# Kernel optimization log

Measured on AMD Instinct MI355X. Metric: run time of the kernel, lower is better.

Reference implementation:

```python
import jax, jax.numpy as jnp
import numpy as np

B, IN, H, G, WR = 8192, 1024, 1024, 2, 64
UR = [64, 64]


def setup_inputs() -> dict:
    key = jax.random.key(0)
    ks = jax.random.split(key, 9)
    hg = H // G
    return {
        "x": jax.random.normal(ks[0], (B, IN), jnp.float32),
        "h": jax.random.normal(ks[1], (B, H), jnp.float32),
        "c": jax.random.normal(ks[2], (B, H), jnp.float32),
        "u_x": 0.1 * jax.random.normal(ks[3], (IN, WR), jnp.float32),
        "v_x": 0.1 * jax.random.normal(ks[4], (4 * H, WR), jnp.float32),
        "u_h_0": 0.1 * jax.random.normal(ks[5], (G, hg, UR[0]), jnp.float32),
        "v_h_0": 0.1 * jax.random.normal(ks[6], (G, UR[0], 4 * hg), jnp.float32),
        "u_h_1": 0.1 * jax.random.normal(ks[7], (G, hg, UR[1]), jnp.float32),
        "v_h_1": 0.1 * jax.random.normal(ks[8], (G, UR[1], 4 * hg), jnp.float32),
        "bias_x": jnp.ones((1, 4 * H), jnp.float32),
        "bias_h": jnp.ones((1, 4 * H), jnp.float32),
    }


def reference(x, h, c, u_x, v_x, u_h_0, v_h_0, u_h_1, v_h_1, bias_x, bias_h):
    b = h.shape[0]
    hg = H // G
    # input-to-hidden low-rank projection: [B, 4H]
    gx = (x @ u_x) @ v_x.T + bias_x
    xf, xi, xn, xo = jnp.split(gx, 4, axis=1)  # each [B, H]

    hv = h.reshape(b, G, hg)  # [B, G, H/G]
    u_hs = [u_h_0, u_h_1]
    v_hs = [v_h_0, v_h_1]
    acc = None
    for i in range(G):
        # torch code rotates the group index list cumulatively each step:
        # step i uses permutation roll(arange(G), -i)
        perm = np.roll(np.arange(G), -i)
        h_op = hv[:, perm, :]  # [B, G, hg]
        t = jnp.einsum('bgd,gdr->bgr', h_op, u_hs[i])  # [B, G, r_i]
        t = jnp.einsum('bgr,grk->bgk', t, v_hs[i])     # [B, G, 4hg]
        acc = t if acc is None else acc + t

    # chunk along last dim into 4 gates, flatten group dim -> [B, H]
    f_h, i_h, n_h, o_h = [p.reshape(b, H) for p in jnp.split(acc, 4, axis=2)]
    hf, hi, hn, ho = jnp.split(bias_h, 4, axis=1)

    inputgate = jax.nn.sigmoid(xi + hi + i_h)
    forgetgate = jax.nn.sigmoid(xf + hf + f_h)
    outputgate = jax.nn.sigmoid(xo + ho + o_h)
    newgate = jnp.tanh(xn + hn + n_h)
    c_next = forgetgate * c + inputgate * newgate
    h_next = outputgate * jnp.tanh(c_next)
    return (h_next, c_next)
```

## Files before the change

kernel.cpp:

```cpp
#include <hip/hip_runtime.h>
#include <hip/hip_bf16.h>


typedef __bf16 bf16_t;
typedef __bf16 bf16x4 __attribute__((ext_vector_type(4)));
typedef __bf16 bf16x8 __attribute__((ext_vector_type(8)));
typedef float f32x4 __attribute__((ext_vector_type(4)));

#define MFMA16x16x32(a, b, c) __builtin_amdgcn_mfma_f32_16x16x32_bf16((a), (b), (c), 0, 0, 0)

#define TA_OFF 0
#define BX_OFF 5242880
#define BH_OFF 5373952
#define BW_OFF 5636096

__device__ inline float fast_sigmoid(float x) {
  return __builtin_amdgcn_rcpf(1.f + __expf(-x));
}
__device__ inline float fast_tanh(float x) {
  return 2.f * __builtin_amdgcn_rcpf(1.f + __expf(-2.f * x)) - 1.f;
}

__global__ __launch_bounds__(256) void prep_kernel(
    const float* __restrict__ u_x, const float* __restrict__ u_h_0,
    const float* __restrict__ u_h_1, const float* __restrict__ v_h_0,
    const float* __restrict__ v_h_1, const float* __restrict__ v_x,
    bf16_t* __restrict__ Bx, bf16_t* __restrict__ Bh,
    bf16_t* __restrict__ Bw) {
  int o = blockIdx.x * 256 + threadIdx.x;
  if (o < 65536) {
    int j = o & 7, lane = (o >> 3) & 63, kk = (o >> 9) & 31, t = o >> 14;
    int lo = lane & 15, quad = lane >> 4;
    int k = kk * 32 + quad * 8 + j;
    Bx[o] = (bf16_t)u_x[k * 64 + 16 * t + lo];
  } else if (o < 196608) {
    int o2 = o - 65536;
    int j = o2 & 7, lane = (o2 >> 3) & 63, kk = (o2 >> 9) & 15;
    int sub = (o2 >> 13) & 3, s = o2 >> 15;
    int lo = lane & 15, quad = lane >> 4;
    int d = kk * 32 + quad * 8 + j;
    const float* src = (s & 1) ? u_h_1 : u_h_0;
    Bh[o2] = (bf16_t)src[(s >> 1) * 32768 + d * 64 + 16 * sub + lo];
  } else if (o < 983040) {
    int o3 = o - 196608;
    int j = o3 & 7, lane = (o3 >> 3) & 63;
    int chunk = o3 >> 9;
    int ks = chunk % 6, rowt = chunk / 6;
    int gq = rowt >> 3, nt = rowt & 7;
    int lo = lane & 15, quad = lane >> 4;
    int g = gq >> 4, qt = gq & 15;
    int row = 16 * nt + lo;
    int w = row >> 5, ql = row & 31;
    int k = ks * 32 + quad * 8 + j;
    int m = g * 512 + qt * 32 + ql;
    int q = qt * 32 + ql;
    float val;
    if (k < 64)
      val = v_x[(w * 1024 + m) * 64 + k];
    else if (k < 128)
      val = v_h_0[g * 131072 + (k - 64) * 2048 + w * 512 + q];
    else
      val = v_h_1[g * 131072 + (k - 128) * 2048 + w * 512 + q];
    Bw[o3] = (bf16_t)val;
  }
}

__global__ __launch_bounds__(256) void phase1_kernel(
    const float* __restrict__ x, const float* __restrict__ h,
    const bf16_t* __restrict__ Bx, const bf16_t* __restrict__ Bh,
    bf16_t* __restrict__ TA) {
  __shared__ bf16_t z[16][1048];
  __shared__ bf16_t pre[16][328];
  const int b0 = blockIdx.x * 16;
  const int tid = threadIdx.x;
  const int wv = tid >> 6, lane = tid & 63;
  const int lo = lane & 15, quad = lane >> 4;
  const int srow = tid >> 4, sc = tid & 15;

  {
    const float* src = x + (size_t)(b0 + srow) * 1024;
#pragma unroll
    for (int j = 0; j < 16; ++j) {
      int col = sc * 4 + j * 64;
      float4 v = *(const float4*)(src + col);
      bf16x4 pk;
      pk[0] = (bf16_t)v.x; pk[1] = (bf16_t)v.y;
      pk[2] = (bf16_t)v.z; pk[3] = (bf16_t)v.w;
      *(bf16x4*)&z[srow][col] = pk;
    }
  }
  __syncthreads();

  {
    f32x4 accx = {0.f, 0.f, 0.f, 0.f};
    const bf16_t* bx = Bx + ((size_t)(wv * 32) * 64 + lane) * 8;
    for (int kk = 0; kk < 32; ++kk) {
      bf16x8 af = *(const bf16x8*)&z[lo][kk * 32 + quad * 8];
      bf16x8 bfr = *(const bf16x8*)(bx + (size_t)kk * 512);
      accx = MFMA16x16x32(af, bfr, accx);
    }
#pragma unroll
    for (int r = 0; r < 4; ++r) pre[quad * 4 + r][16 * wv + lo] = (bf16_t)accx[r];
  }
  __syncthreads();

  {
    const float* src = h + (size_t)(b0 + srow) * 1024;
#pragma unroll
    for (int j = 0; j < 16; ++j) {
      int col = sc * 4 + j * 64;
      float4 v = *(const float4*)(src + col);
      bf16x4 pk;
      pk[0] = (bf16_t)v.x; pk[1] = (bf16_t)v.y;
      pk[2] = (bf16_t)v.z; pk[3] = (bf16_t)v.w;
      *(bf16x4*)&z[srow][col] = pk;
    }
  }
  __syncthreads();

  {
    const int hoff = (wv == 1 || wv == 2) ? 512 : 0;
    f32x4 acc[4];
#pragma unroll
    for (int sub = 0; sub < 4; ++sub) acc[sub] = (f32x4){0.f, 0.f, 0.f, 0.f};
    for (int kk = 0; kk < 16; ++kk) {
      bf16x8 af = *(const bf16x8*)&z[lo][hoff + kk * 32 + quad * 8];
#pragma unroll
      for (int sub = 0; sub < 4; ++sub) {
        bf16x8 bfr = *(const bf16x8*)(Bh +
            (((size_t)(wv * 4 + sub) * 16 + kk) * 64 + lane) * 8);
        acc[sub] = MFMA16x16x32(af, bfr, acc[sub]);
      }
    }
#pragma unroll
    for (int sub = 0; sub < 4; ++sub) {
      int n = 64 + wv * 64 + sub * 16 + lo;
#pragma unroll
      for (int r = 0; r < 4; ++r) pre[quad * 4 + r][n] = (bf16_t)acc[sub][r];
    }
  }
  __syncthreads();

#pragma unroll
  for (int it = 0; it < 3; ++it) {
    int slot = it * 256 + tid;
    if (slot < 640) {
      int cc = slot >> 6, ln = slot & 63;
      int llo = ln & 15, lq = ln >> 4;
      bf16x8 v = *(const bf16x8*)&pre[llo][cc * 32 + lq * 8];
      *(bf16x8*)(TA + (((size_t)blockIdx.x * 10 + cc) * 64 + ln) * 8) = v;
    }
  }
}

__global__ __launch_bounds__(256, 3) void phase2_kernel(
    const bf16_t* __restrict__ TA, const bf16_t* __restrict__ Bw,
    const float* __restrict__ bias_x, const float* __restrict__ bias_h,
    const float* __restrict__ c, float* __restrict__ out) {
  const int b0 = blockIdx.x * 128;
  const int gq = blockIdx.y;
  const int g = gq >> 4, qt = gq & 15;
  const int tid = threadIdx.x;
  const int wv = tid >> 6, lane = tid & 63;
  const int lo = lane & 15, quad = lane >> 4;

  bf16x8 a[2][6];
#pragma unroll
  for (int mt = 0; mt < 2; ++mt) {
    int rt = blockIdx.x * 8 + wv * 2 + mt;
#pragma unroll
    for (int ks = 0; ks < 6; ++ks) {
      int cc = (ks < 2) ? ks : (g * 4 + ks);
      a[mt][ks] = *(const bf16x8*)(TA + (((size_t)rt * 10 + cc) * 64 + lane) * 8);
    }
  }

  float bsum[4][2];
#pragma unroll
  for (int w = 0; w < 4; ++w)
#pragma unroll
    for (int cq = 0; cq < 2; ++cq) {
      int n = w * 1024 + g * 512 + qt * 32 + cq * 16 + lo;
      bsum[w][cq] = bias_x[n] + bias_h[n];
    }

  f32x4 acc[2][8];
#pragma unroll
  for (int mt = 0; mt < 2; ++mt)
#pragma unroll
    for (int nt = 0; nt < 8; ++nt) acc[mt][nt] = (f32x4){0.f, 0.f, 0.f, 0.f};

#pragma unroll
  for (int nt = 0; nt < 8; ++nt) {
#pragma unroll
    for (int ks = 0; ks < 6; ++ks) {
      bf16x8 bfr = *(const bf16x8*)(Bw +
          (((size_t)(gq * 8 + nt) * 6 + ks) * 64 + lane) * 8);
      acc[0][nt] = MFMA16x16x32(a[0][ks], bfr, acc[0][nt]);
      acc[1][nt] = MFMA16x16x32(a[1][ks], bfr, acc[1][nt]);
    }
  }

#pragma unroll
  for (int mt = 0; mt < 2; ++mt)
#pragma unroll
    for (int r = 0; r < 4; ++r) {
      int b = b0 + wv * 32 + mt * 16 + quad * 4 + r;
#pragma unroll
      for (int cq = 0; cq < 2; ++cq) {
        int m = g * 512 + qt * 32 + cq * 16 + lo;
        float fv = acc[mt][0 + cq][r] + bsum[0][cq];
        float iv = acc[mt][2 + cq][r] + bsum[1][cq];
        float nv = acc[mt][4 + cq][r] + bsum[2][cq];
        float ov = acc[mt][6 + cq][r] + bsum[3][cq];
        float cin = c[(size_t)b * 1024 + m];
        float ig = fast_sigmoid(iv);
        float fg = fast_sigmoid(fv);
        float og = fast_sigmoid(ov);
        float ng = fast_tanh(nv);
        float cn = fg * cin + ig * ng;
        float hn = og * fast_tanh(cn);
        out[(size_t)b * 1024 + m] = hn;
        out[8388608ull + (size_t)b * 1024 + m] = cn;
      }
    }
}

extern "C" void kernel_launch(void* const* d_in, const int* in_sizes, int n_in,
                              void* d_out, int out_size, void* d_ws,
                              size_t ws_size, hipStream_t stream) {
  const float* x = (const float*)d_in[0];
  const float* h = (const float*)d_in[1];
  const float* c = (const float*)d_in[2];
  const float* u_x = (const float*)d_in[3];
  const float* v_x = (const float*)d_in[4];
  const float* u_h_0 = (const float*)d_in[5];
  const float* v_h_0 = (const float*)d_in[6];
  const float* u_h_1 = (const float*)d_in[7];
  const float* v_h_1 = (const float*)d_in[8];
  const float* bias_x = (const float*)d_in[9];
  const float* bias_h = (const float*)d_in[10];

  char* ws = (char*)d_ws;
  bf16_t* TA = (bf16_t*)(ws + TA_OFF);
  bf16_t* Bx = (bf16_t*)(ws + BX_OFF);
  bf16_t* Bh = (bf16_t*)(ws + BH_OFF);
  bf16_t* Bw = (bf16_t*)(ws + BW_OFF);

  prep_kernel<<<3840, 256, 0, stream>>>(u_x, u_h_0, u_h_1, v_h_0, v_h_1, v_x,
                                        Bx, Bh, Bw);
  phase1_kernel<<<512, 256, 0, stream>>>(x, h, Bx, Bh, TA);
  phase2_kernel<<<dim3(64, 32), 256, 0, stream>>>(TA, Bw, bias_x, bias_h, c,
                                                  (float*)d_out);
}
```

Measured before the change: 205.9 us.

## Stage B weights in LDS, prefetch c, and merge x/h loads in phase1

Phase1 now loads and converts both x and h into a doubled shared buffer up front, which removes two barriers and lets the h loads overlap the x projection. Phase2 copies the per-group Bw slice (48 KB) into shared memory cooperatively, so it is no longer re-read from global memory inside the MFMA loop. It also prefetches the c values before the matmul so their latency is hidden. The cost is more shared memory per block, which may lower occupancy in both kernels, plus extra register pressure from holding the prefetched c values.

```diff
diff --git a/kernel.cpp b/kernel.cpp
--- a/kernel.cpp
+++ b/kernel.cpp
@@ -69,7 +69,7 @@
     const float* __restrict__ x, const float* __restrict__ h,
     const bf16_t* __restrict__ Bx, const bf16_t* __restrict__ Bh,
     bf16_t* __restrict__ TA) {
-  __shared__ bf16_t z[16][1048];
+  __shared__ bf16_t z[16][2072];
   __shared__ bf16_t pre[16][328];
   const int b0 = blockIdx.x * 16;
   const int tid = threadIdx.x;
@@ -78,15 +78,25 @@
   const int srow = tid >> 4, sc = tid & 15;
 
   {
-    const float* src = x + (size_t)(b0 + srow) * 1024;
+    const float* srcx = x + (size_t)(b0 + srow) * 1024;
+    const float* srch = h + (size_t)(b0 + srow) * 1024;
 #pragma unroll
     for (int j = 0; j < 16; ++j) {
       int col = sc * 4 + j * 64;
-      float4 v = *(const float4*)(src + col);
+      float4 v = *(const float4*)(srcx + col);
       bf16x4 pk;
       pk[0] = (bf16_t)v.x; pk[1] = (bf16_t)v.y;
       pk[2] = (bf16_t)v.z; pk[3] = (bf16_t)v.w;
       *(bf16x4*)&z[srow][col] = pk;
+    }
+#pragma unroll
+    for (int j = 0; j < 16; ++j) {
+      int col = sc * 4 + j * 64;
+      float4 v = *(const float4*)(srch + col);
+      bf16x4 pk;
+      pk[0] = (bf16_t)v.x; pk[1] = (bf16_t)v.y;
+      pk[2] = (bf16_t)v.z; pk[3] = (bf16_t)v.w;
+      *(bf16x4*)&z[srow][1024 + col] = pk;
     }
   }
   __syncthreads();
@@ -102,24 +112,9 @@
 #pragma unroll
     for (int r = 0; r < 4; ++r) pre[quad * 4 + r][16 * wv + lo] = (bf16_t)accx[r];
   }
-  __syncthreads();
-
-  {
-    const float* src = h + (size_t)(b0 + srow) * 1024;
-#pragma unroll
-    for (int j = 0; j < 16; ++j) {
-      int col = sc * 4 + j * 64;
-      float4 v = *(const float4*)(src + col);
-      bf16x4 pk;
-      pk[0] = (bf16_t)v.x; pk[1] = (bf16_t)v.y;
-      pk[2] = (bf16_t)v.z; pk[3] = (bf16_t)v.w;
-      *(bf16x4*)&z[srow][col] = pk;
-    }
-  }
-  __syncthreads();
-
-  {
-    const int hoff = (wv == 1 || wv == 2) ? 512 : 0;
+
+  {
+    const int hoff = 1024 + ((wv == 1 || wv == 2) ? 512 : 0);
     f32x4 acc[4];
 #pragma unroll
     for (int sub = 0; sub < 4; ++sub) acc[sub] = (f32x4){0.f, 0.f, 0.f, 0.f};
@@ -157,6 +152,8 @@
     const bf16_t* __restrict__ TA, const bf16_t* __restrict__ Bw,
     const float* __restrict__ bias_x, const float* __restrict__ bias_h,
     const float* __restrict__ c, float* __restrict__ out) {
+  __shared__ bf16_t bs[3072 * 8];
+
   const int b0 = blockIdx.x * 128;
   const int gq = blockIdx.y;
   const int g = gq >> 4, qt = gq & 15;
@@ -175,6 +172,27 @@
     }
   }
 
+  {
+    const bf16_t* src = Bw + (size_t)gq * 24576;
+#pragma unroll
+    for (int cch = 0; cch < 12; ++cch) {
+      int ch = cch * 256 + tid;
+      *(bf16x8*)&bs[(size_t)ch * 8] = *(const bf16x8*)(src + (size_t)ch * 8);
+    }
+  }
+
+  float cin[2][4][2];
+#pragma unroll
+  for (int mt = 0; mt < 2; ++mt)
+#pragma unroll
+    for (int r = 0; r < 4; ++r) {
+      int b = b0 + wv * 32 + mt * 16 + quad * 4 + r;
+#pragma unroll
+      for (int cq = 0; cq < 2; ++cq) {
+        int m = g * 512 + qt * 32 + cq * 16 + lo;
+        cin[mt][r][cq] = c[(size_t)b * 1024 + m];
+      }
+    }
   float bsum[4][2];
 #pragma unroll
   for (int w = 0; w < 4; ++w)
@@ -183,6 +201,7 @@
       int n = w * 1024 + g * 512 + qt * 32 + cq * 16 + lo;
       bsum[w][cq] = bias_x[n] + bias_h[n];
     }
+  __syncthreads();
 
   f32x4 acc[2][8];
 #pragma unroll
@@ -194,8 +213,7 @@
   for (int nt = 0; nt < 8; ++nt) {
 #pragma unroll
     for (int ks = 0; ks < 6; ++ks) {
-      bf16x8 bfr = *(const bf16x8*)(Bw +
-          (((size_t)(gq * 8 + nt) * 6 + ks) * 64 + lane) * 8);
+      bf16x8 bfr = *(const bf16x8*)&bs[(size_t)(((nt * 6 + ks) << 6) + lane) * 8];
       acc[0][nt] = MFMA16x16x32(a[0][ks], bfr, acc[0][nt]);
       acc[1][nt] = MFMA16x16x32(a[1][ks], bfr, acc[1][nt]);
     }
@@ -213,12 +231,11 @@
         float iv = acc[mt][2 + cq][r] + bsum[1][cq];
         float nv = acc[mt][4 + cq][r] + bsum[2][cq];
         float ov = acc[mt][6 + cq][r] + bsum[3][cq];
-        float cin = c[(size_t)b * 1024 + m];
         float ig = fast_sigmoid(iv);
         float fg = fast_sigmoid(fv);
         float og = fast_sigmoid(ov);
         float ng = fast_tanh(nv);
-        float cn = fg * cin + ig * ng;
+        float cn = fg * cin[mt][r][cq] + ig * ng;
         float hn = og * fast_tanh(cn);
         out[(size_t)b * 1024 + m] = hn;
         out[8388608ull + (size_t)b * 1024 + m] = cn;
```

After: 191.5 us. 1.08x faster.
